# Kernel optimization log

Hardware: AMD Instinct MI355X
Metric: run time of the kernel (lower is better)

The kernel has to match this reference:

```python
import jax, jax.numpy as jnp
import numpy as np

BSZ, H, P, L = 8, 512, 128, 8192
DT_MIN, DT_MAX = 1e-3, 1e-1


def setup_inputs() -> dict:
    key = jax.random.key(0)
    ks = jax.random.split(key, 6)
    inp = {}
    inp["input_sequence"] = jax.random.normal(ks[0], (BSZ, 1, H, 1, L), jnp.float32)
    # HiPPO-like init: negative real parts, pi*k imaginary parts
    inp["Lambda_re"] = -jax.random.uniform(ks[1], (P,), jnp.float32, 0.1, 1.0)
    inp["Lambda_im"] = jnp.pi * jnp.arange(P, dtype=jnp.float32)
    # lecun_normal-ish: fan_in = H for B, fan_in = P for C (real+imag parts)
    inp["B"] = jax.random.normal(ks[2], (P, H, 2), jnp.float32) / np.float32(np.sqrt(2 * H))
    inp["C"] = jax.random.normal(ks[3], (H, P, 2), jnp.float32) / np.float32(np.sqrt(2 * P))
    inp["D"] = jax.random.normal(ks[4], (H,), jnp.float32)
    u01 = jax.random.uniform(ks[5], (P, 1), jnp.float32)
    inp["log_step"] = u01 * np.float32(np.log(DT_MAX) - np.log(DT_MIN)) + np.float32(np.log(DT_MIN))
    return inp


def _binary_operator(q_i, q_j):
    A_i, b_i = q_i
    A_j, b_j = q_j
    return (A_j * A_i, A_j * b_i + b_j)


def reference(input_sequence, Lambda_re, Lambda_im, B, C, D, log_step):
    # (bsz, 1, H, 1, L) -> (bsz, L, H)
    u = input_sequence[:, 0, :, 0].transpose(0, 2, 1)

    Lambda = Lambda_re + 1j * Lambda_im                      # (P,)
    B_tilde = B[..., 0] + 1j * B[..., 1]                     # (P, H)
    C_tilde = C[..., 0] + 1j * C[..., 1]                     # (H, P)
    step = jnp.exp(log_step[:, 0])                           # (P,)

    # zero-order hold discretization
    Lambda_bar = jnp.exp(Lambda * step)                      # (P,)
    B_bar = ((Lambda_bar - 1.0) / Lambda)[:, None] * B_tilde # (P, H)

    Bu = jnp.einsum('blh,ph->blp', u, B_bar)                 # (bsz, L, P) complex
    Lambda_elems = jnp.broadcast_to(Lambda_bar, Bu.shape)
    _, xs = jax.lax.associative_scan(_binary_operator, (Lambda_elems, Bu), axis=1)

    # conj_sym=True -> factor of 2 on the real part of emissions
    ys = 2.0 * jnp.einsum('blp,hp->blh', xs, C_tilde).real + D * u
    ys = jax.nn.gelu(ys, approximate=False)

    # back to (bsz, 1, H, 1, L)
    return ys.transpose(0, 2, 1)[:, None, :, None, :]
```

## Files before the change

kernel.cpp:

```cpp
#include <hip/hip_runtime.h>
#include <hip/hip_bf16.h>
#include <cmath>

namespace {
constexpr int Pn = 128;
constexpr int Hn = 512;
constexpr int Ln = 8192;
constexpr int BS = 8;
constexpr size_t OFF_BMAT = 2048;
constexpr size_t OFF_CMAT = 264192;
constexpr size_t OFF_PPOW = 526336;
constexpr size_t OFF_END  = 591872;
constexpr size_t OFF_CAR  = 1640448;
constexpr size_t HEADB    = 2689024;
constexpr size_t SZ_BU = (size_t)256 * Ln * 2;
}

typedef __attribute__((ext_vector_type(4))) float f32x4;
typedef __attribute__((ext_vector_type(8))) short bf16x8;

static __device__ inline short f2bf(float x) {
  __hip_bfloat16 h = __float2bfloat16(x);
  return *(short*)&h;
}
static __device__ inline float bf2f(short s) {
  unsigned u = ((unsigned)(unsigned short)s) << 16;
  return __uint_as_float(u);
}

static __device__ inline void async_copy16(const void* g, void* l) {
  __builtin_amdgcn_global_load_lds(
      (const __attribute__((address_space(1))) unsigned int*)g,
      (__attribute__((address_space(3))) unsigned int*)l, 16, 0, 0);
}

__global__ void precompute_kernel(const float* __restrict__ Lre,
                                  const float* __restrict__ Lim,
                                  const float* __restrict__ Bin,
                                  const float* __restrict__ Cin,
                                  const float* __restrict__ lstep,
                                  float* __restrict__ Lam,
                                  __hip_bfloat16* __restrict__ Bmat,
                                  __hip_bfloat16* __restrict__ Cmat,
                                  float* __restrict__ Ppow) {
  int tid = blockIdx.x * blockDim.x + threadIdx.x;
  if (tid < 2 * Pn * Hn) {
    int r = tid >> 9;
    int h = tid & (Hn - 1);
    int p = r & (Pn - 1);
    float st = expf(lstep[p]);
    float lr = Lre[p], li = Lim[p];
    float er = expf(lr * st);
    float cr = er * cosf(li * st);
    float ci = er * sinf(li * st);
    float nr = cr - 1.0f, ni = ci;
    float inv = 1.0f / (lr * lr + li * li);
    float wr = (nr * lr + ni * li) * inv;
    float wi = (ni * lr - nr * li) * inv;
    float btr = Bin[(p * Hn + h) * 2 + 0];
    float bti = Bin[(p * Hn + h) * 2 + 1];
    float val = (r < Pn) ? (wr * btr - wi * bti) : (wr * bti + wi * btr);
    Bmat[tid] = __float2bfloat16(val);
  } else if (tid < 4 * Pn * Hn) {
    int j = tid - 2 * Pn * Hn;
    int h = j >> 8;
    int c = j & 255;
    int p = c & (Pn - 1);
    float v = (c < Pn) ? 2.0f * Cin[(h * Pn + p) * 2 + 0]
                       : -2.0f * Cin[(h * Pn + p) * 2 + 1];
    Cmat[j] = __float2bfloat16(v);
  } else if (tid < 4 * Pn * Hn + 512) {
    int j = tid - 4 * Pn * Hn;
    int p = j & 127;
    int sel = j >> 7;
    float st = expf(lstep[p]);
    float lr = Lre[p], li = Lim[p];
    float sc = (sel < 2) ? st : 64.0f * st;
    float er = expf(lr * sc);
    Lam[(sel >> 1) * 256 + (sel & 1) * 128 + p] =
        (sel & 1) ? er * sinf(li * sc) : er * cosf(li * sc);
  } else if (tid < 4 * Pn * Hn + 512 + 64 * 256) {
    int j = tid - 4 * Pn * Hn - 512;
    int jr = j >> 8;
    int k = j & 255;
    int p = k & 127;
    float st = expf(lstep[p]);
    float lr = Lre[p], li = Lim[p];
    float tt = st * (float)(jr + 1);
    float er = expf(lr * tt);
    Ppow[j] = (k < 128) ? er * cosf(li * tt) : er * sinf(li * tt);
  }
}

__global__ __launch_bounds__(256) void gemm1_kernel(
    const __hip_bfloat16* __restrict__ Amat,
    const float* __restrict__ U,
    short* __restrict__ Bu,
    float* __restrict__ End,
    const float* __restrict__ Lam,
    int b0) {
  __shared__ __align__(16) char shm[33280];
  short* As = (short*)shm;
  short* Bsb = (short*)(shm + 16384);
  float (*Sl)[260] = (float(*)[260])shm;
  const int t = threadIdx.x;
  const int lane = t & 63, w = t >> 6;
  const int n0 = blockIdx.x * 64;
  const int bz = blockIdx.z;
  const float* Ub = U + (size_t)(b0 + bz) * Hn * Ln;

  const int srow = lane >> 2, scol = (lane & 3) * 16;
  const int bn = t & 63, bkg = t >> 6;
  const int lr = lane & 15, lk = (lane >> 4) * 8;

  f32x4 acc[4][4] = {};
  for (int k0 = 0; k0 < Hn; k0 += 32) {
#pragma unroll
    for (int I2 = 0; I2 < 4; I2++) {
      int I = 4 * w + I2;
      async_copy16((const char*)(Amat + (size_t)(16 * I + srow) * Hn + k0) + scol,
                   (char*)As + I * 1024);
    }
    {
      float v[8];
#pragma unroll
      for (int j = 0; j < 8; j++)
        v[j] = Ub[(size_t)(k0 + bkg * 8 + j) * Ln + n0 + bn];
      bf16x8 pk;
#pragma unroll
      for (int j = 0; j < 8; j++) pk[j] = f2bf(v[j]);
      *(bf16x8*)&Bsb[bn * 40 + bkg * 8] = pk;
    }
    __syncthreads();
    bf16x8 af[4], bfr[4];
#pragma unroll
    for (int mt = 0; mt < 4; mt++)
      af[mt] = *(const bf16x8*)&As[(64 * w + 16 * mt + lr) * 32 + lk];
#pragma unroll
    for (int nt = 0; nt < 4; nt++)
      bfr[nt] = *(const bf16x8*)&Bsb[(16 * nt + lr) * 40 + lk];
#pragma unroll
    for (int mt = 0; mt < 4; mt++)
#pragma unroll
      for (int nt = 0; nt < 4; nt++)
        acc[mt][nt] = __builtin_amdgcn_mfma_f32_16x16x32_bf16(
            af[mt], bfr[nt], acc[mt][nt], 0, 0, 0);
    __syncthreads();
  }

  const int row4 = (lane >> 4) * 4, col = lane & 15;
  short* Bub = Bu + (size_t)bz * Ln * 256;
  float scr = 0.f, sci = 0.f;
  const float Ar = Lam[t & 127], Ai = Lam[128 + (t & 127)];
#pragma unroll
  for (int pass = 0; pass < 2; pass++) {
    __syncthreads();
#pragma unroll
    for (int mt = 0; mt < 4; mt++)
#pragma unroll
      for (int ntl = 0; ntl < 2; ntl++) {
        int nt = 2 * pass + ntl;
        *(f32x4*)&Sl[16 * ntl + col][64 * w + 16 * mt + row4] = acc[mt][nt];
      }
    __syncthreads();
    if (t < 128) {
      const int p = t;
#pragma unroll
      for (int j = 0; j < 32; j++) {
        float br = Sl[j][p], bi = Sl[j][128 + p];
        float nr = fmaf(Ar, scr, fmaf(-Ai, sci, br));
        float ni = fmaf(Ar, sci, fmaf(Ai, scr, bi));
        scr = nr; sci = ni;
        Sl[j][p] = nr; Sl[j][128 + p] = ni;
      }
    }
    __syncthreads();
    {
      const int row = t >> 3, seg = t & 7;
      short* dst = Bub + (size_t)(n0 + 32 * pass + row) * 256 + seg * 32;
      const float* src = &Sl[row][seg * 32];
#pragma unroll
      for (int q = 0; q < 4; q++) {
        bf16x8 pk;
#pragma unroll
        for (int j = 0; j < 8; j++) pk[j] = f2bf(src[8 * q + j]);
        *(bf16x8*)&dst[8 * q] = pk;
      }
    }
  }
  if (t < 128) {
    float* E = End + ((size_t)bz * 128 + blockIdx.x) * 256;
    E[t] = scr;
    E[128 + t] = sci;
  }
}

__global__ __launch_bounds__(128) void carry_kernel(const float* __restrict__ End,
                                                    float* __restrict__ Carry,
                                                    const float* __restrict__ Lam) {
  const int bz = blockIdx.x;
  const int p = threadIdx.x;
  const float a64r = Lam[256 + p], a64i = Lam[384 + p];
  const float* E = End + (size_t)bz * 128 * 256;
  float* C = Carry + (size_t)bz * 128 * 256;
  float xr = 0.f, xi = 0.f;
  float er0[4], ei0[4], er1[4], ei1[4];
#pragma unroll
  for (int q = 0; q < 4; q++) {
    er0[q] = E[(size_t)q * 256 + p];
    ei0[q] = E[(size_t)q * 256 + 128 + p];
  }
  for (int c0 = 0; c0 < 128; c0 += 8) {
#pragma unroll
    for (int q = 0; q < 4; q++) {
      er1[q] = E[(size_t)(c0 + 4 + q) * 256 + p];
      ei1[q] = E[(size_t)(c0 + 4 + q) * 256 + 128 + p];
    }
#pragma unroll
    for (int q = 0; q < 4; q++) {
      C[(size_t)(c0 + q) * 256 + p] = xr;
      C[(size_t)(c0 + q) * 256 + 128 + p] = xi;
      float nr = fmaf(a64r, xr, fmaf(-a64i, xi, er0[q]));
      float ni = fmaf(a64r, xi, fmaf(a64i, xr, ei0[q]));
      xr = nr; xi = ni;
    }
#pragma unroll
    for (int q = 0; q < 4; q++) {
      int cn = c0 + 8 + q;
      if (cn < 128) {
        er0[q] = E[(size_t)cn * 256 + p];
        ei0[q] = E[(size_t)cn * 256 + 128 + p];
      }
    }
#pragma unroll
    for (int q = 0; q < 4; q++) {
      C[(size_t)(c0 + 4 + q) * 256 + p] = xr;
      C[(size_t)(c0 + 4 + q) * 256 + 128 + p] = xi;
      float nr = fmaf(a64r, xr, fmaf(-a64i, xi, er1[q]));
      float ni = fmaf(a64r, xi, fmaf(a64i, xr, ei1[q]));
      xr = nr; xi = ni;
    }
  }
}

__global__ __launch_bounds__(256) void gemm2_kernel(
    const __hip_bfloat16* __restrict__ Cmat,
    const short* __restrict__ Xs,
    const float* __restrict__ Ppow,
    const float* __restrict__ Cy,
    const float* __restrict__ U,
    const float* __restrict__ Dv,
    float* __restrict__ Out, int b0) {
  __shared__ __align__(16) short As[2][128 * 32];
  __shared__ __align__(16) short Bs[2][128 * 40];
  __shared__ __align__(16) float CyS[512];
  const int t = threadIdx.x;
  const int lane = t & 63, w = t >> 6;
  const int wm = w >> 1, wn = w & 1;
  const int n0 = blockIdx.x * 128;
  const int m0 = blockIdx.y * 128;
  const int bz = blockIdx.z;
  const int b = b0 + bz;

  const int srow = lane >> 2, scol = (lane & 3) * 16;
  const int krow = t >> 2, kq = t & 3;
  const short* Xb = Xs + ((size_t)bz * Ln + n0) * 256;

  bf16x8 xl[2];
  f32x4 Pr[4];

  auto STAGE_A = [&](int s, int buf) {
    const int k0 = s * 32;
#pragma unroll
    for (int I2 = 0; I2 < 2; I2++) {
      int I = 2 * w + I2;
      async_copy16((const char*)(Cmat + (size_t)(m0 + 16 * I + srow) * 256 + k0) + scol,
                   (char*)As[buf] + I * 1024);
    }
  };
  auto STAGE_ISSUE = [&](int s) {
    const int kwin = s * 32 + kq * 8;
    const int p0 = kwin & 127;
#pragma unroll
    for (int ro = 0; ro < 2; ro++)
      xl[ro] = *(const bf16x8*)&Xb[(size_t)(ro * 64 + krow) * 256 + kwin];
    Pr[0] = *(const f32x4*)&Ppow[krow * 256 + p0];
    Pr[1] = *(const f32x4*)&Ppow[krow * 256 + p0 + 4];
    Pr[2] = *(const f32x4*)&Ppow[krow * 256 + 128 + p0];
    Pr[3] = *(const f32x4*)&Ppow[krow * 256 + 128 + p0 + 4];
  };
  auto STAGE_WRITE = [&](int s, int buf) {
    const int kwin = s * 32 + kq * 8;
    const bool isRe = kwin < 128;
    const int p0 = kwin & 127;
    const int ha = isRe ? 0 : 128, hb = isRe ? 128 : 0;
#pragma unroll
    for (int ro = 0; ro < 2; ro++) {
      f32x4 u0 = *(const f32x4*)&CyS[ro * 256 + ha + p0];
      f32x4 u1 = *(const f32x4*)&CyS[ro * 256 + ha + p0 + 4];
      f32x4 v0 = *(const f32x4*)&CyS[ro * 256 + hb + p0];
      f32x4 v1 = *(const f32x4*)&CyS[ro * 256 + hb + p0 + 4];
      if (isRe) { v0 = -v0; v1 = -v1; }
      bf16x8 pk;
#pragma unroll
      for (int q = 0; q < 4; q++) {
        float v = fmaf(Pr[0][q], u0[q], fmaf(Pr[2][q], v0[q], bf2f(xl[ro][q])));
        pk[q] = f2bf(v);
      }
#pragma unroll
      for (int q = 0; q < 4; q++) {
        float v = fmaf(Pr[1][q], u1[q], fmaf(Pr[3][q], v1[q], bf2f(xl[ro][4 + q])));
        pk[4 + q] = f2bf(v);
      }
      *(bf16x8*)&Bs[buf][(ro * 64 + krow) * 40 + kq * 8] = pk;
    }
  };

  STAGE_A(0, 0);
  STAGE_ISSUE(0);
  {
    const float* Cyb = Cy + ((size_t)bz * 128 + (n0 >> 6)) * 256;
    CyS[t] = Cyb[t];
    CyS[256 + t] = Cyb[256 + t];
  }
  __syncthreads();
  STAGE_WRITE(0, 0);
  __syncthreads();

  const int lr = lane & 15, lk = (lane >> 4) * 8;
  f32x4 acc[4][4] = {};
#pragma unroll
  for (int s = 0; s < 8; s++) {
    const int cur = s & 1;
    if (s < 7) {
      STAGE_A(s + 1, cur ^ 1);
      STAGE_ISSUE(s + 1);
    }
    bf16x8 af[4], bfr[4];
#pragma unroll
    for (int mt = 0; mt < 4; mt++)
      af[mt] = *(const bf16x8*)&As[cur][(64 * wm + 16 * mt + lr) * 32 + lk];
#pragma unroll
    for (int nt = 0; nt < 4; nt++)
      bfr[nt] = *(const bf16x8*)&Bs[cur][(64 * wn + 16 * nt + lr) * 40 + lk];
#pragma unroll
    for (int mt = 0; mt < 4; mt++)
#pragma unroll
      for (int nt = 0; nt < 4; nt++)
        acc[mt][nt] = __builtin_amdgcn_mfma_f32_16x16x32_bf16(
            af[mt], bfr[nt], acc[mt][nt], 0, 0, 0);
    if (s < 7) STAGE_WRITE(s + 1, cur ^ 1);
    __syncthreads();
  }

  const int row4 = (lane >> 4) * 4, col = lane & 15;
#pragma unroll
  for (int mt = 0; mt < 4; mt++) {
#pragma unroll
    for (int r = 0; r < 4; r++) {
      int h = m0 + 64 * wm + 16 * mt + row4 + r;
      float dh = Dv[h];
      const float* Urow = U + ((size_t)b * Hn + h) * Ln;
      float* Orow = Out + ((size_t)b * Hn + h) * Ln;
#pragma unroll
      for (int nt = 0; nt < 4; nt++) {
        int n = n0 + 64 * wn + 16 * nt + col;
        float y = acc[mt][nt][r] + dh * Urow[n];
        float u2 = y * (0.7978845608f + 0.0356774081f * y * y);
        Orow[n] = y / (1.0f + __expf(-2.0f * u2));
      }
    }
  }
}

extern "C" void kernel_launch(void* const* d_in, const int* in_sizes, int n_in,
                              void* d_out, int out_size, void* d_ws, size_t ws_size,
                              hipStream_t stream) {
  const float* U   = (const float*)d_in[0];
  const float* Lre = (const float*)d_in[1];
  const float* Lim = (const float*)d_in[2];
  const float* Bin = (const float*)d_in[3];
  const float* Cin = (const float*)d_in[4];
  const float* Dv  = (const float*)d_in[5];
  const float* ls  = (const float*)d_in[6];
  float* out = (float*)d_out;

  char* wsb = (char*)d_ws;
  float* Lam = (float*)wsb;
  __hip_bfloat16* Bmat = (__hip_bfloat16*)(wsb + OFF_BMAT);
  __hip_bfloat16* Cmat = (__hip_bfloat16*)(wsb + OFF_CMAT);
  float* Ppow = (float*)(wsb + OFF_PPOW);
  float* End = (float*)(wsb + OFF_END);
  float* Cy  = (float*)(wsb + OFF_CAR);
  short* Bu  = (short*)(wsb + HEADB);

  int NB = 8;
  while (NB > 1 && ws_size < HEADB + (size_t)NB * SZ_BU)
    NB >>= 1;

  precompute_kernel<<<(4 * Pn * Hn + 512 + 64 * 256 + 255) / 256, 256, 0, stream>>>(
      Lre, Lim, Bin, Cin, ls, Lam, Bmat, Cmat, Ppow);

  for (int b0 = 0; b0 < BS; b0 += NB) {
    gemm1_kernel<<<dim3(Ln / 64, 1, NB), 256, 0, stream>>>(Bmat, U, Bu, End, Lam, b0);
    carry_kernel<<<dim3(NB), 128, 0, stream>>>(End, Cy, Lam);
    gemm2_kernel<<<dim3(Ln / 128, Hn / 128, NB), 256, 0, stream>>>(
        Cmat, Bu, Ppow, Cy, U, Dv, out, b0);
  }
}
```

Measured before the change: 335.3 us.

## Double-buffer gemm1 shared-memory tiles to overlap loads with MFMA

Converts the gemm1 K-loop to a double-buffered pipeline. The next A tile is staged asynchronously and the next U slice is loaded into registers while MFMAs run on the current buffer. The converted U slice is written to the alternate buffer afterwards, so only one barrier per iteration remains. This hides global-load latency at the cost of more LDS (43 KB instead of 33 KB), extra registers and a fully unrolled 16-step loop, which may reduce occupancy.

```diff
diff --git a/kernel.cpp b/kernel.cpp
--- a/kernel.cpp
+++ b/kernel.cpp
@@ -99,9 +99,9 @@
     float* __restrict__ End,
     const float* __restrict__ Lam,
     int b0) {
-  __shared__ __align__(16) char shm[33280];
-  short* As = (short*)shm;
-  short* Bsb = (short*)(shm + 16384);
+  __shared__ __align__(16) char shm[43008];
+  short* As0 = (short*)shm;
+  short* Bs0 = (short*)(shm + 32768);
   float (*Sl)[260] = (float(*)[260])shm;
   const int t = threadIdx.x;
   const int lane = t & 63, w = t >> 6;
@@ -113,38 +113,54 @@
   const int bn = t & 63, bkg = t >> 6;
   const int lr = lane & 15, lk = (lane >> 4) * 8;
 
-  f32x4 acc[4][4] = {};
-  for (int k0 = 0; k0 < Hn; k0 += 32) {
+  float v[8];
+  auto STAGE_A = [&](int k0, int buf) {
 #pragma unroll
     for (int I2 = 0; I2 < 4; I2++) {
       int I = 4 * w + I2;
       async_copy16((const char*)(Amat + (size_t)(16 * I + srow) * Hn + k0) + scol,
-                   (char*)As + I * 1024);
-    }
-    {
-      float v[8];
-#pragma unroll
-      for (int j = 0; j < 8; j++)
-        v[j] = Ub[(size_t)(k0 + bkg * 8 + j) * Ln + n0 + bn];
-      bf16x8 pk;
-#pragma unroll
-      for (int j = 0; j < 8; j++) pk[j] = f2bf(v[j]);
-      *(bf16x8*)&Bsb[bn * 40 + bkg * 8] = pk;
-    }
-    __syncthreads();
+                   (char*)As0 + buf * 16384 + I * 1024);
+    }
+  };
+  auto U_ISSUE = [&](int k0) {
+#pragma unroll
+    for (int j = 0; j < 8; j++)
+      v[j] = Ub[(size_t)(k0 + bkg * 8 + j) * Ln + n0 + bn];
+  };
+  auto U_WRITE = [&](int buf) {
+    bf16x8 pk;
+#pragma unroll
+    for (int j = 0; j < 8; j++) pk[j] = f2bf(v[j]);
+    *(bf16x8*)&Bs0[buf * 2560 + bn * 40 + bkg * 8] = pk;
+  };
+
+  STAGE_A(0, 0);
+  U_ISSUE(0);
+  U_WRITE(0);
+  __syncthreads();
+
+  f32x4 acc[4][4] = {};
+#pragma unroll
+  for (int s = 0; s < 16; s++) {
+    const int cur = s & 1;
+    if (s < 15) {
+      STAGE_A((s + 1) * 32, cur ^ 1);
+      U_ISSUE((s + 1) * 32);
+    }
     bf16x8 af[4], bfr[4];
 #pragma unroll
     for (int mt = 0; mt < 4; mt++)
-      af[mt] = *(const bf16x8*)&As[(64 * w + 16 * mt + lr) * 32 + lk];
+      af[mt] = *(const bf16x8*)&As0[cur * 8192 + (64 * w + 16 * mt + lr) * 32 + lk];
 #pragma unroll
     for (int nt = 0; nt < 4; nt++)
-      bfr[nt] = *(const bf16x8*)&Bsb[(16 * nt + lr) * 40 + lk];
+      bfr[nt] = *(const bf16x8*)&Bs0[cur * 2560 + (16 * nt + lr) * 40 + lk];
 #pragma unroll
     for (int mt = 0; mt < 4; mt++)
 #pragma unroll
       for (int nt = 0; nt < 4; nt++)
         acc[mt][nt] = __builtin_amdgcn_mfma_f32_16x16x32_bf16(
             af[mt], bfr[nt], acc[mt][nt], 0, 0, 0);
+    if (s < 15) U_WRITE(cur ^ 1);
     __syncthreads();
   }
 
```

After: 336.6 us. No clear change (+0.4%).
